# Performance work log

Measured on AMD Instinct MI355X. Metric: run time of the kernel, lower is better.

The kernel has to match this reference:

```python
import jax, jax.numpy as jnp
import numpy as np

N = 8192      # number of nodes
D = 16        # inp_dim (forced by W: [16,18])
DH = 18       # GAT hidden dim (forced by W/a)
H = 8         # num_heads


def setup_inputs() -> dict:
    key = jax.random.key(0)
    k1, k2, k3, k4 = jax.random.split(key, 4)
    inputs = jax.random.normal(k1, (N, D), dtype=jnp.float32)
    # xavier-ish init scale for W (torch uses xavier_uniform gain=1.414)
    W = jax.random.normal(k2, (D, DH), dtype=jnp.float32) * np.float32(np.sqrt(2.0 / (D + DH)) * 1.414)
    a = jax.random.normal(k3, (2 * DH, 1), dtype=jnp.float32) * np.float32(0.1)
    Wk = jax.random.normal(k4, (H, D, D), dtype=jnp.float32)  # stacked attention_wts_k
    return {"inputs": inputs, "W": W, "a": a, "Wk": Wk}


def reference(inputs, W, a, Wk):
    # h = inputs @ W  -> [N, 18]
    h = jnp.matmul(inputs, W)
    # a_input[i, j] = concat(h[i], h[j]); score e[i,j] = a_input[i,j] @ a.
    # Decompose instead of materializing [N*N, 36]:
    #   e[i,j] = h[i] @ a[:18] + h[j] @ a[18:]
    a1 = a[:DH, 0]  # [18]
    a2 = a[DH:, 0]  # [18]
    e = (h @ a1)[:, None] + (h @ a2)[None, :]        # [N, N]
    # softmax over dim=-2 of [N, N, 1] == axis 1 of [N, N] (neighbor axis)
    score = jax.nn.softmax(e, axis=1)                # [N, N]
    # per-head linear: op1[h] = inputs @ Wk[h]  -> [H, N, 16]
    op1 = jnp.einsum('nd,hde->hne', inputs, Wk)
    # scored_x sum over neighbors: out[i,h,:] = sum_j score[i,j] * op1[h,j,:]
    out = jnp.einsum('nm,hmd->nhd', score, op1)      # [N, H, 16]
    return out.reshape(N, H * D)                     # concat heads -> [N, 128]
```

## Files before the change

### kernel.cpp

```cpp
#include <hip/hip_runtime.h>

#define N 8192
#define D 16
#define DH 18
#define H 8

typedef float v4f __attribute__((ext_vector_type(4)));

__global__ __launch_bounds__(256) void attn_fused(
        const float* __restrict__ x, const float* __restrict__ W,
        const float* __restrict__ a, const float* __restrict__ Wk,
        float* __restrict__ out) {
    __shared__ float w2[D];
    __shared__ float part[4][D + 1];
    __shared__ float sv[D + 1];
    __shared__ float ov[H * D];
    const int t = threadIdx.x;

    if (t < D) {
        float s = 0.f;
        #pragma unroll
        for (int j = 0; j < DH; ++j) s += W[t * DH + j] * a[DH + j];
        w2[t] = s;
    }
    __syncthreads();

    float w2r[D];
    #pragma unroll
    for (int d = 0; d < D; ++d) w2r[d] = w2[d];

    float acc[D + 1];
    #pragma unroll
    for (int k = 0; k < D + 1; ++k) acc[k] = 0.f;

    const v4f* xp = reinterpret_cast<const v4f*>(x);
    #pragma unroll 4
    for (int r = 0; r < N / 256; ++r) {
        const int m = r * 256 + t;
        v4f q0 = xp[m * 4 + 0];
        v4f q1 = xp[m * 4 + 1];
        v4f q2 = xp[m * 4 + 2];
        v4f q3 = xp[m * 4 + 3];
        float xv[D];
        xv[0]=q0.x;  xv[1]=q0.y;  xv[2]=q0.z;  xv[3]=q0.w;
        xv[4]=q1.x;  xv[5]=q1.y;  xv[6]=q1.z;  xv[7]=q1.w;
        xv[8]=q2.x;  xv[9]=q2.y;  xv[10]=q2.z; xv[11]=q2.w;
        xv[12]=q3.x; xv[13]=q3.y; xv[14]=q3.z; xv[15]=q3.w;

        float g = 0.f;
        #pragma unroll
        for (int d = 0; d < D; ++d) g += xv[d] * w2r[d];
        const float w = expf(g);

        acc[0] += w;
        #pragma unroll
        for (int d = 0; d < D; ++d) acc[1 + d] += w * xv[d];
    }

    #pragma unroll
    for (int off = 32; off > 0; off >>= 1) {
        #pragma unroll
        for (int k = 0; k < D + 1; ++k)
            acc[k] += __shfl_down(acc[k], off, 64);
    }
    const int wave = t >> 6, lane = t & 63;
    if (lane == 0) {
        #pragma unroll
        for (int k = 0; k < D + 1; ++k) part[wave][k] = acc[k];
    }
    __syncthreads();
    if (t < D + 1)
        sv[t] = part[0][t] + part[1][t] + part[2][t] + part[3][t];
    __syncthreads();

    if (t < H * D) {
        const int h = t >> 4, e = t & 15;
        const float inv = 1.0f / sv[0];
        float s = 0.f;
        #pragma unroll
        for (int d = 0; d < D; ++d)
            s += sv[1 + d] * Wk[h * (D * D) + d * D + e];
        ov[t] = s * inv;
    }
    __syncthreads();

    const v4f* ov4 = reinterpret_cast<const v4f*>(ov);
    v4f* out4 = reinterpret_cast<v4f*>(out);
    const v4f val = ov4[t & 31];
    const int base = blockIdx.x * 1024 + t;
    #pragma unroll
    for (int i = 0; i < 4; ++i)
        __builtin_nontemporal_store(val, &out4[base + i * 256]);
}

extern "C" void kernel_launch(void* const* d_in, const int* in_sizes, int n_in,
                              void* d_out, int out_size, void* d_ws, size_t ws_size,
                              hipStream_t stream) {
    const float* inputs = (const float*)d_in[0];
    const float* W      = (const float*)d_in[1];
    const float* a      = (const float*)d_in[2];
    const float* Wk     = (const float*)d_in[3];
    float* out = (float*)d_out;

    attn_fused<<<256, 256, 0, stream>>>(inputs, W, a, Wk, out);
}
```

Baseline: 72.56 us.

## Split column reduction across blocks with cooperative grid sync

Previously every block redundantly reduced all 8192 rows to get the softmax-weighted column sums. Now 32 blocks each reduce 256 rows and write partial sums to workspace. A cooperative grid sync follows, then every block combines the partials and writes its output slice. This removes the redundant per-block loop over all rows, at the cost of a grid-wide barrier and a cooperative launch.

```diff
diff --git a/kernel.cpp b/kernel.cpp
--- a/kernel.cpp
+++ b/kernel.cpp
@@ -1,46 +1,40 @@
 #include <hip/hip_runtime.h>
+#include <hip/hip_cooperative_groups.h>
+
+namespace cg = cooperative_groups;
 
 #define N 8192
 #define D 16
 #define DH 18
 #define H 8
+#define PBLK 32
+#define GRID 256
 
 typedef float v4f __attribute__((ext_vector_type(4)));
 
-__global__ __launch_bounds__(256) void attn_fused(
+__global__ __launch_bounds__(256) void attn_coop(
         const float* __restrict__ x, const float* __restrict__ W,
         const float* __restrict__ a, const float* __restrict__ Wk,
-        float* __restrict__ out) {
+        float* __restrict__ out, float* __restrict__ ws) {
     __shared__ float w2[D];
     __shared__ float part[4][D + 1];
     __shared__ float sv[D + 1];
     __shared__ float ov[H * D];
     const int t = threadIdx.x;
+    const int b = blockIdx.x;
 
-    if (t < D) {
-        float s = 0.f;
-        #pragma unroll
-        for (int j = 0; j < DH; ++j) s += W[t * DH + j] * a[DH + j];
-        w2[t] = s;
-    }
-    __syncthreads();
+    if (b < PBLK) {
+        if (t < D) {
+            float s = 0.f;
+            #pragma unroll
+            for (int j = 0; j < DH; ++j) s += W[t * DH + j] * a[DH + j];
+            w2[t] = s;
+        }
+        __syncthreads();
 
-    float w2r[D];
-    #pragma unroll
-    for (int d = 0; d < D; ++d) w2r[d] = w2[d];
-
-    float acc[D + 1];
-    #pragma unroll
-    for (int k = 0; k < D + 1; ++k) acc[k] = 0.f;
-
-    const v4f* xp = reinterpret_cast<const v4f*>(x);
-    #pragma unroll 4
-    for (int r = 0; r < N / 256; ++r) {
-        const int m = r * 256 + t;
-        v4f q0 = xp[m * 4 + 0];
-        v4f q1 = xp[m * 4 + 1];
-        v4f q2 = xp[m * 4 + 2];
-        v4f q3 = xp[m * 4 + 3];
+        const int m = b * 256 + t;
+        const v4f* xp = reinterpret_cast<const v4f*>(x + (size_t)m * D);
+        v4f q0 = xp[0], q1 = xp[1], q2 = xp[2], q3 = xp[3];
         float xv[D];
         xv[0]=q0.x;  xv[1]=q0.y;  xv[2]=q0.z;  xv[3]=q0.w;
         xv[4]=q1.x;  xv[5]=q1.y;  xv[6]=q1.z;  xv[7]=q1.w;
@@ -49,30 +43,43 @@
 
         float g = 0.f;
         #pragma unroll
-        for (int d = 0; d < D; ++d) g += xv[d] * w2r[d];
+        for (int d = 0; d < D; ++d) g += xv[d] * w2[d];
         const float w = expf(g);
 
-        acc[0] += w;
+        float acc[D + 1];
+        acc[0] = w;
         #pragma unroll
-        for (int d = 0; d < D; ++d) acc[1 + d] += w * xv[d];
+        for (int d = 0; d < D; ++d) acc[1 + d] = w * xv[d];
+
+        #pragma unroll
+        for (int off = 32; off > 0; off >>= 1) {
+            #pragma unroll
+            for (int k = 0; k < D + 1; ++k)
+                acc[k] += __shfl_down(acc[k], off, 64);
+        }
+        const int wave = t >> 6, lane = t & 63;
+        if (lane == 0) {
+            #pragma unroll
+            for (int k = 0; k < D + 1; ++k) part[wave][k] = acc[k];
+        }
+        __syncthreads();
+        if (t < D + 1) {
+            float s = part[0][t] + part[1][t] + part[2][t] + part[3][t];
+            ws[t * PBLK + b] = s;
+        }
+        __threadfence();
     }
 
-    #pragma unroll
-    for (int off = 32; off > 0; off >>= 1) {
+    cg::this_grid().sync();
+
+    if (t < D + 1) {
+        const v4f* wsv = reinterpret_cast<const v4f*>(ws + t * PBLK);
+        v4f s4 = wsv[0];
         #pragma unroll
-        for (int k = 0; k < D + 1; ++k)
-            acc[k] += __shfl_down(acc[k], off, 64);
-    }
-    const int wave = t >> 6, lane = t & 63;
-    if (lane == 0) {
-        #pragma unroll
-        for (int k = 0; k < D + 1; ++k) part[wave][k] = acc[k];
+        for (int j = 1; j < PBLK / 4; ++j) s4 += wsv[j];
+        sv[t] = s4.x + s4.y + s4.z + s4.w;
     }
     __syncthreads();
-    if (t < D + 1)
-        sv[t] = part[0][t] + part[1][t] + part[2][t] + part[3][t];
-    __syncthreads();
-
     if (t < H * D) {
         const int h = t >> 4, e = t & 15;
         const float inv = 1.0f / sv[0];
@@ -84,10 +91,9 @@
     }
     __syncthreads();
 
-    const v4f* ov4 = reinterpret_cast<const v4f*>(ov);
+    const v4f val = reinterpret_cast<const v4f*>(ov)[t & 31];
     v4f* out4 = reinterpret_cast<v4f*>(out);
-    const v4f val = ov4[t & 31];
-    const int base = blockIdx.x * 1024 + t;
+    const int base = b * 1024 + t;
     #pragma unroll
     for (int i = 0; i < 4; ++i)
         __builtin_nontemporal_store(val, &out4[base + i * 256]);
@@ -101,6 +107,10 @@
     const float* a      = (const float*)d_in[2];
     const float* Wk     = (const float*)d_in[3];
     float* out = (float*)d_out;
+    float* ws  = (float*)d_ws;
 
-    attn_fused<<<256, 256, 0, stream>>>(inputs, W, a, Wk, out);
+    void* args[] = { (void*)&inputs, (void*)&W, (void*)&a, (void*)&Wk,
+                     (void*)&out, (void*)&ws };
+    hipLaunchCooperativeKernel((const void*)attn_coop, dim3(GRID), dim3(256),
+                               args, 0, stream);
 }
```

After: 101.0 us. +39.3%, slower.
